# Performance work log

Hardware: AMD Instinct MI355X
Metric: run time of the kernel (lower is better)

The kernel has to match this reference:

```python
import jax, jax.numpy as jnp
import numpy as np

B, T, V, D, H, L = 256, 256, 128, 384, 6, 6
HS = D // H  # 64
FF = 4 * D


def _ln(x, g, b):
    m = jnp.mean(x, axis=-1, keepdims=True)
    v = jnp.var(x, axis=-1, keepdims=True)
    return (x - m) / jnp.sqrt(v + 1e-5) * g + b


def setup_inputs() -> dict:
    key = jax.random.key(0)
    ks = jax.random.split(key, 16)
    s = lambda k, sh: jax.random.normal(k, sh, dtype=jnp.float32) * 0.02
    return {
        "idx": jax.random.randint(ks[0], (B, T), 0, V),
        "tok_emb": s(ks[1], (V, D)),
        "pos_emb": s(ks[2], (T, D)),
        "Wq": s(ks[3], (L, H, D, HS)),
        "Wk": s(ks[4], (L, H, D, HS)),
        "Wv": s(ks[5], (L, H, D, HS)),
        "Wproj": s(ks[6], (L, D, D)),
        "bproj": jnp.zeros((L, D), jnp.float32),
        "ln1_g": jnp.ones((L, D), jnp.float32),
        "ln1_b": jnp.zeros((L, D), jnp.float32),
        "ln2_g": jnp.ones((L, D), jnp.float32),
        "ln2_b": jnp.zeros((L, D), jnp.float32),
        "W1": s(ks[7], (L, D, FF)),
        "b1": jnp.zeros((L, FF), jnp.float32),
        "W2": s(ks[8], (L, FF, D)),
        "b2": jnp.zeros((L, D), jnp.float32),
        "lnf_g": jnp.ones((D,), jnp.float32),
        "lnf_b": jnp.zeros((D,), jnp.float32),
        "Wlm": s(ks[9], (D, V)),
        "blm": jnp.zeros((V,), jnp.float32),
    }


def reference(idx, tok_emb, pos_emb, Wq, Wk, Wv, Wproj, bproj,
              ln1_g, ln1_b, ln2_g, ln2_b, W1, b1, W2, b2,
              lnf_g, lnf_b, Wlm, blm):
    Bv, Tv = idx.shape
    x = tok_emb[idx] + pos_emb[:Tv]  # [B,T,D]
    mask = jnp.tril(jnp.ones((Tv, Tv), dtype=bool))
    scale = HS ** -0.5
    for l in range(L):
        xn = _ln(x, ln1_g[l], ln1_b[l])
        q = jnp.einsum('btd,hdk->bhtk', xn, Wq[l])
        k = jnp.einsum('btd,hdk->bhtk', xn, Wk[l])
        v = jnp.einsum('btd,hdk->bhtk', xn, Wv[l])
        wei = jnp.einsum('bhtk,bhsk->bhts', q, k) * scale  # [B,H,T,T]
        wei = jnp.where(mask, wei, -jnp.inf)
        wei = jax.nn.softmax(wei, axis=-1)
        o = jnp.einsum('bhts,bhsk->bhtk', wei, v)
        o = o.transpose(0, 2, 1, 3).reshape(Bv, Tv, D)  # concat heads
        x = x + o @ Wproj[l] + bproj[l]
        xn = _ln(x, ln2_g[l], ln2_b[l])
        x = x + jax.nn.relu(xn @ W1[l] + b1[l]) @ W2[l] + b2[l]
    x = _ln(x, lnf_g, lnf_b)
    return x @ Wlm + blm  # logits [B,T,V]
```

## Files before the change

kernel.cpp:

```cpp
#include <hip/hip_runtime.h>
#include <stdint.h>

typedef unsigned short u16;
typedef __attribute__((ext_vector_type(8))) short short8;
typedef __attribute__((ext_vector_type(4))) float floatx4;

#define BB 256
#define TT 256
#define VOC 128
#define DD 384
#define HH 6
#define LLAY 6
#define HS 64
#define FFF 1536
#define BT (BB*TT)

__device__ __forceinline__ float b2f(u16 u) {
  union { float f; uint32_t i; } x; x.i = ((uint32_t)u) << 16; return x.f;
}
__device__ __forceinline__ u16 f2b(float f) {
  union { float f; uint32_t i; } x; x.f = f;
  uint32_t r = x.i + 0x7fffu + ((x.i >> 16) & 1u);
  return (u16)(r >> 16);
}
__device__ __forceinline__ float ldf(const void* p, size_t i, int bf) {
  return bf ? b2f(((const u16*)p)[i]) : ((const float*)p)[i];
}
__device__ __forceinline__ int get_bf(const u16* probe) {
  return probe[0] == 0x3F80;
}

__device__ __forceinline__ void gl2lds16(const u16* g, u16* l) {
  __builtin_amdgcn_global_load_lds(
      (const __attribute__((address_space(1))) unsigned int*)g,
      (__attribute__((address_space(3))) unsigned int*)l, 16, 0, 0);
}

__global__ __launch_bounds__(256) void k_repack_qkv(
    const void* __restrict__ Wq, const void* __restrict__ Wk,
    const void* __restrict__ Wv, u16* __restrict__ out,
    const void* __restrict__ g1, const void* __restrict__ b1n,
    float* __restrict__ u, float* __restrict__ v, const u16* probe) {
  __shared__ float t[32][33];
  int bf = get_bf(probe);
  int z = blockIdx.z;
  int h = z % 6, ls = z / 6, sel = ls % 3, l = ls / 3;
  const void* W = sel == 0 ? Wq : (sel == 1 ? Wk : Wv);
  int c0 = blockIdx.x * 32;
  int r0 = blockIdx.y * 32;
  int tx = threadIdx.x & 31, ty = threadIdx.x >> 5;
#pragma unroll
  for (int i = 0; i < 32; i += 8)
    t[ty + i][tx] = ldf(W, (((size_t)(l * 6 + h)) * 384 + r0 + ty + i) * 64 + c0 + tx, bf);
  __syncthreads();
  float gv = ldf(g1, (size_t)l * 384 + r0 + tx, bf);
  float bv = ldf(b1n, (size_t)l * 384 + r0 + tx, bf);
#pragma unroll
  for (int i = 0; i < 32; i += 8) {
    float w = t[tx][ty + i];
    int n = sel * 384 + h * 64 + c0 + ty + i;
    out[((size_t)l * 1152 + n) * 384 + r0 + tx] = f2b(w * gv);
    float pu = w * gv, pv = w * bv;
#pragma unroll
    for (int m = 1; m < 32; m <<= 1) { pu += __shfl_xor(pu, m); pv += __shfl_xor(pv, m); }
    if (tx == 0) {
      atomicAdd(&u[(size_t)l * 1152 + n], pu);
      atomicAdd(&v[(size_t)l * 1152 + n], pv);
    }
  }
}

__global__ __launch_bounds__(256) void k_transpose(
    const void* __restrict__ in, u16* __restrict__ out, int R, int C,
    const u16* probe) {
  __shared__ float t[32][33];
  int bf = get_bf(probe);
  int c0 = blockIdx.x * 32, r0 = blockIdx.y * 32, l = blockIdx.z;
  int tx = threadIdx.x & 31, ty = threadIdx.x >> 5;
  size_t base = (size_t)l * R * C;
#pragma unroll
  for (int i = 0; i < 32; i += 8)
    t[ty + i][tx] = ldf(in, base + (size_t)(r0 + ty + i) * C + c0 + tx, bf);
  __syncthreads();
#pragma unroll
  for (int i = 0; i < 32; i += 8)
    out[base + (size_t)(c0 + ty + i) * R + r0 + tx] = f2b(t[tx][ty + i]);
}

__global__ __launch_bounds__(256) void k_transpose_ln(
    const void* __restrict__ in, u16* __restrict__ out, int R, int C,
    const void* __restrict__ g, const void* __restrict__ b,
    float* __restrict__ u, float* __restrict__ v, const u16* probe) {
  __shared__ float t[32][33];
  int bf = get_bf(probe);
  int c0 = blockIdx.x * 32, r0 = blockIdx.y * 32, l = blockIdx.z;
  int tx = threadIdx.x & 31, ty = threadIdx.x >> 5;
  size_t base = (size_t)l * R * C;
#pragma unroll
  for (int i = 0; i < 32; i += 8)
    t[ty + i][tx] = ldf(in, base + (size_t)(r0 + ty + i) * C + c0 + tx, bf);
  __syncthreads();
  float gv = ldf(g, (size_t)l * R + r0 + tx, bf);
  float bv = ldf(b, (size_t)l * R + r0 + tx, bf);
#pragma unroll
  for (int i = 0; i < 32; i += 8) {
    float w = t[tx][ty + i];
    out[base + (size_t)(c0 + ty + i) * R + r0 + tx] = f2b(w * gv);
    float pu = w * gv, pv = w * bv;
#pragma unroll
    for (int m = 1; m < 32; m <<= 1) { pu += __shfl_xor(pu, m); pv += __shfl_xor(pv, m); }
    if (tx == 0) {
      atomicAdd(&u[(size_t)l * C + c0 + ty + i], pu);
      atomicAdd(&v[(size_t)l * C + c0 + ty + i], pv);
    }
  }
}

__global__ __launch_bounds__(256) void k_embed(
    const int* __restrict__ idx, const void* __restrict__ tok,
    const void* __restrict__ pos, u16* __restrict__ X,
    float* __restrict__ st, const u16* probe) {
  int bf = get_bf(probe);
  int gw = (blockIdx.x * 256 + threadIdx.x) >> 6;
  int lane = threadIdx.x & 63;
  int nw = (gridDim.x * 256) >> 6;
  for (int row = gw; row < BT; row += nw) {
    int v = idx[row];
    size_t tb = (size_t)v * DD, pb = (size_t)(row & 255) * DD;
    u16* xr = X + (size_t)row * DD;
    float s = 0.f, ss = 0.f;
#pragma unroll
    for (int i = 0; i < 6; ++i) {
      int d = i * 64 + lane;
      float x = ldf(tok, tb + d, bf) + ldf(pos, pb + d, bf);
      u16 xb = f2b(x);
      xr[d] = xb;
      float v2 = b2f(xb);
      s += v2; ss += v2 * v2;
    }
#pragma unroll
    for (int m = 1; m < 64; m <<= 1) { s += __shfl_xor(s, m); ss += __shfl_xor(ss, m); }
    if (lane == 0) {
      float mean = s * (1.f / DD);
      float var = ss * (1.f / DD) - mean * mean;
      st[2 * row] = mean;
      st[2 * row + 1] = rsqrtf(var + 1e-5f);
    }
  }
}

__global__ __launch_bounds__(256) void k_finstats(
    const float* __restrict__ stp, float* __restrict__ st) {
  int r = blockIdx.x * 256 + threadIdx.x;
  const float* p = stp + (size_t)r * 12;
  float s = 0.f, ss = 0.f;
#pragma unroll
  for (int k = 0; k < 6; ++k) { s += p[2 * k]; ss += p[2 * k + 1]; }
  float mean = s * (1.f / DD);
  float var = ss * (1.f / DD) - mean * mean;
  st[2 * r] = mean;
  st[2 * r + 1] = rsqrtf(var + 1e-5f);
}

template <int EPI>
__global__ __launch_bounds__(512) void k_gemm(
    const u16* __restrict__ A, const u16* __restrict__ Bt,
    const void* __restrict__ bias, int boff, u16* __restrict__ Xb,
    u16* __restrict__ C, float* __restrict__ Cf, int N, int K,
    const float* __restrict__ st, const float* __restrict__ u,
    const float* __restrict__ v, float* __restrict__ stp,
    const u16* probe) {
  __shared__ u16 As[256 * 64];
  __shared__ u16 Bs[128 * 64];
  int tid = threadIdx.x, lane = tid & 63, wave = tid >> 6;
  int m0 = blockIdx.x * 256, n0 = blockIdx.y * 128;
  int srow = tid >> 3;
  int skg = ((tid & 7) ^ (srow & 7)) * 8;
  const u16* gA = A + (size_t)(m0 + srow) * K + skg;
  const u16* gB = Bt + (size_t)(n0 + srow) * K + skg;
  u16* lA = As + wave * 512;
  u16* lB = Bs + wave * 512;
  int wy = wave >> 1, wx = wave & 1;
  int lr = lane & 15, quad = lane >> 4;
  int sx = lr & 7;
  floatx4 acc[4][4];
#pragma unroll
  for (int i = 0; i < 4; ++i)
#pragma unroll
    for (int j = 0; j < 4; ++j) acc[i][j] = (floatx4){0.f, 0.f, 0.f, 0.f};

  const u16* Abase = As + (size_t)(wy * 64 + lr) * 64;
  const u16* Bbase = Bs + (size_t)(wx * 64 + lr) * 64;

  int nk = K >> 6;
  for (int bk = 0; bk < nk; ++bk) {
    __syncthreads();
#pragma unroll
    for (int c = 0; c < 4; ++c)
      gl2lds16(gA + (size_t)(c * 64) * K, lA + c * 4096);
#pragma unroll
    for (int c = 0; c < 2; ++c)
      gl2lds16(gB + (size_t)(c * 64) * K, lB + c * 4096);
    gA += 64; gB += 64;
    __syncthreads();
#pragma unroll
    for (int half = 0; half < 2; ++half) {
      int ko = ((quad + half * 4) ^ sx) * 8;
      short8 af[4], bfr[4];
#pragma unroll
      for (int i = 0; i < 4; ++i) af[i] = *(const short8*)(Abase + i * 1024 + ko);
#pragma unroll
      for (int j = 0; j < 4; ++j) bfr[j] = *(const short8*)(Bbase + j * 1024 + ko);
#pragma unroll
      for (int i = 0; i < 4; ++i)
#pragma unroll
        for (int j = 0; j < 4; ++j)
          acc[i][j] = __builtin_amdgcn_mfma_f32_16x16x32_bf16(af[i], bfr[j], acc[i][j], 0, 0, 0);
    }
  }

  if (EPI == 2) {
    int bfl = get_bf(probe);
    float bv2[4];
#pragma unroll
    for (int j = 0; j < 4; ++j)
      bv2[j] = ldf(bias, boff + n0 + wx * 64 + j * 16 + lr, bfl);
    int slot = blockIdx.y * 2 + wx;
#pragma unroll
    for (int i = 0; i < 4; ++i) {
      int mrow = m0 + wy * 64 + i * 16 + quad * 4;
#pragma unroll
      for (int r = 0; r < 4; ++r) {
        int grow = mrow + r;
        float s = 0.f, ss = 0.f;
#pragma unroll
        for (int j = 0; j < 4; ++j) {
          int n = n0 + wx * 64 + j * 16 + lr;
          size_t off = (size_t)grow * N + n;
          u16 val = f2b(b2f(Xb[off]) + acc[i][j][r] + bv2[j]);
          Xb[off] = val;
          float yr = b2f(val);
          s += yr; ss += yr * yr;
        }
#pragma unroll
        for (int m = 1; m < 16; m <<= 1) { s += __shfl_xor(s, m); ss += __shfl_xor(ss, m); }
        if (lr == 0) {
          float2 pr; pr.x = s; pr.y = ss;
          *(float2*)(stp + ((size_t)grow * 6 + slot) * 2) = pr;
        }
      }
    }
  } else {
    int bfl = (EPI == 1 || EPI == 3) ? get_bf(probe) : 1;
    float un[4], vn[4], bv[4], sc[4];
    size_t sb[4]; int nc[4];
#pragma unroll
    for (int j = 0; j < 4; ++j) {
      int n = n0 + wx * 64 + j * 16 + lr;
      un[j] = u[n]; vn[j] = v[n];
      bv[j] = (EPI == 4) ? 0.f : ldf(bias, boff + n, bfl);
      sc[j] = 1.f;
      if (EPI == 4) {
        int sel = n >= 768 ? 2 : (n >= 384 ? 1 : 0);
        int hh = (n - sel * 384) >> 6;
        sb[j] = (size_t)sel * boff * 384 + (size_t)hh * boff * 64;
        nc[j] = n & 63;
        if (sel == 0) sc[j] = 0.125f;
      }
    }
#pragma unroll
    for (int i = 0; i < 4; ++i) {
      int mrow = m0 + wy * 64 + i * 16 + quad * 4;
#pragma unroll
      for (int r = 0; r < 4; ++r) {
        int grow = mrow + r;
        float mu = st[2 * grow], rs = st[2 * grow + 1];
#pragma unroll
        for (int j = 0; j < 4; ++j) {
          int n = n0 + wx * 64 + j * 16 + lr;
          float y = rs * (acc[i][j][r] - mu * un[j]) + vn[j];
          if (EPI == 1) C[(size_t)grow * N + n] = f2b(fmaxf(y + bv[j], 0.f));
          else if (EPI == 3) {
            if (bfl) C[(size_t)grow * N + n] = f2b(y + bv[j]);
            else Cf[(size_t)grow * N + n] = y + bv[j];
          } else {
            C[sb[j] + (size_t)grow * 64 + nc[j]] = f2b(y * sc[j]);
          }
        }
      }
    }
  }
}

__global__ __launch_bounds__(256) void k_attn(
    const u16* __restrict__ Q, const u16* __restrict__ K,
    const u16* __restrict__ V, u16* __restrict__ O, int TB) {
  __shared__ u16 Vt[2][64 * 72];
  __shared__ u16 P[4 * 16 * 72];
  int bx = blockIdx.x;
  int h = blockIdx.y;
  int b = blockIdx.z;
  int tid = threadIdx.x, lane = tid & 63, wave = tid >> 6;
  int lr = lane & 15, quad = lane >> 4;
  size_t hbase = (size_t)h * TB;
  const u16* Vb = V + (hbase + b * TT) * 64;

  int sp = tid & 31, sc = tid >> 5;

  {
    const u16* v0 = Vb + (size_t)(2 * sp) * 64 + sc * 8;
    short8 a = *(const short8*)(v0);
    short8 bvv = *(const short8*)(v0 + 64);
#pragma unroll
    for (int e = 0; e < 8; ++e) {
      uint32_t pk = (uint32_t)(u16)a[e] | ((uint32_t)(u16)bvv[e] << 16);
      *(uint32_t*)&Vt[0][(sc * 8 + e) * 72 + 2 * sp] = pk;
    }
  }

  int t0w = bx * 64 + wave * 16;
  const u16* qrow = Q + (hbase + b * TT + t0w + lr) * 64 + quad * 8;
  short8 qf0 = *(const short8*)(qrow);
  short8 qf1 = *(const short8*)(qrow + 32);

  float ls[4];
  floatx4 oacc[4];
#pragma unroll
  for (int r = 0; r < 4; ++r) ls[r] = 0.f;
#pragma unroll
  for (int j2 = 0; j2 < 4; ++j2) oacc[j2] = (floatx4){0.f, 0.f, 0.f, 0.f};
  u16* Pw = P + wave * 1152;
  const u16* Pr = P + wave * 1152 + lr * 72 + quad * 8;

  __syncthreads();

  for (int ks = 0; ks <= bx; ++ks) {
    short8 sva, svb;
    bool do_stage = (ks < bx);
    if (do_stage) {
      const u16* v0 = Vb + (size_t)((ks + 1) * 64 + 2 * sp) * 64 + sc * 8;
      sva = *(const short8*)(v0);
      svb = *(const short8*)(v0 + 64);
    }

    floatx4 s[4];
#pragma unroll
    for (int cc = 0; cc < 4; ++cc) s[cc] = (floatx4){0.f, 0.f, 0.f, 0.f};
    const u16* kbase = K + (hbase + b * TT + ks * 64 + lr) * 64 + quad * 8;
#pragma unroll
    for (int cc = 0; cc < 4; ++cc) {
      const u16* kr = kbase + cc * 16 * 64;
      short8 kf;
      kf = *(const short8*)(kr);      s[cc] = __builtin_amdgcn_mfma_f32_16x16x32_bf16(qf0, kf, s[cc], 0, 0, 0);
      kf = *(const short8*)(kr + 32); s[cc] = __builtin_amdgcn_mfma_f32_16x16x32_bf16(qf1, kf, s[cc], 0, 0, 0);
    }

    if (ks == bx) {
#pragma unroll
      for (int r = 0; r < 4; ++r) {
        int rowt = t0w + quad * 4 + r;
#pragma unroll
        for (int cc = 0; cc < 4; ++cc) {
          int c = ks * 64 + cc * 16 + lr;
          float e = (c > rowt) ? 0.f : __expf(s[cc][r]);
          ls[r] += e;
          Pw[(quad * 4 + r) * 72 + cc * 16 + lr] = f2b(e);
        }
      }
    } else {
#pragma unroll
      for (int r = 0; r < 4; ++r)
#pragma unroll
        for (int cc = 0; cc < 4; ++cc) {
          float e = __expf(s[cc][r]);
          ls[r] += e;
          Pw[(quad * 4 + r) * 72 + cc * 16 + lr] = f2b(e);
        }
    }
    asm volatile("s_waitcnt lgkmcnt(0)" ::: "memory");
    const u16* Vc = &Vt[ks & 1][0];
#pragma unroll
    for (int h2 = 0; h2 < 2; ++h2) {
      short8 pf = *(const short8*)(Pr + h2 * 32);
#pragma unroll
      for (int j2 = 0; j2 < 4; ++j2) {
        short8 vf = *(const short8*)(Vc + (j2 * 16 + lr) * 72 + h2 * 32 + quad * 8);
        oacc[j2] = __builtin_amdgcn_mfma_f32_16x16x32_bf16(pf, vf, oacc[j2], 0, 0, 0);
      }
    }

    if (do_stage) {
      u16* dst = &Vt[(ks + 1) & 1][0];
#pragma unroll
      for (int e = 0; e < 8; ++e) {
        uint32_t pk = (uint32_t)(u16)sva[e] | ((uint32_t)(u16)svb[e] << 16);
        *(uint32_t*)&dst[(sc * 8 + e) * 72 + 2 * sp] = pk;
      }
    }
    __syncthreads();
  }

#pragma unroll
  for (int r = 0; r < 4; ++r) {
#pragma unroll
    for (int mm = 1; mm < 16; mm <<= 1) ls[r] += __shfl_xor(ls[r], mm);
    ls[r] = 1.f / ls[r];
  }

  u16* Ot = (u16*)Vt;
#pragma unroll
  for (int j2 = 0; j2 < 4; ++j2)
#pragma unroll
    for (int r = 0; r < 4; ++r)
      Ot[(wave * 16 + quad * 4 + r) * 72 + j2 * 16 + lr] = f2b(oacc[j2][r] * ls[r]);
  __syncthreads();
#pragma unroll
  for (int p = 0; p < 2; ++p) {
    int row = p * 32 + (tid >> 3), cg = tid & 7;
    short8 o8 = *(const short8*)(Ot + row * 72 + cg * 8);
    *(short8*)(O + (size_t)(b * TT + bx * 64 + row) * DD + h * 64 + cg * 8) = o8;
  }
}

extern "C" void kernel_launch(void* const* d_in, const int* in_sizes, int n_in,
                              void* d_out, int out_size, void* d_ws, size_t ws_size,
                              hipStream_t stream) {
  const int* idx   = (const int*)d_in[0];
  const void* tok  = d_in[1];
  const void* pos  = d_in[2];
  const void* Wq   = d_in[3];
  const void* Wk   = d_in[4];
  const void* Wv   = d_in[5];
  const void* Wproj= d_in[6];
  const void* bproj= d_in[7];
  const void* ln1g = d_in[8];
  const void* ln1b = d_in[9];
  const void* ln2g = d_in[10];
  const void* ln2b = d_in[11];
  const void* W1   = d_in[12];
  const void* b1   = d_in[13];
  const void* W2   = d_in[14];
  const void* b2   = d_in[15];
  const void* lnfg = d_in[16];
  const void* lnfb = d_in[17];
  const void* Wlm  = d_in[18];
  const void* blm  = d_in[19];
  const u16* probe = (const u16*)d_in[8];

  char* ws = (char*)d_ws;
  u16* X  = (u16*)ws;
  u16* XA = (u16*)(ws + 50331648);
  char* wb = ws + 100663296;
  u16* Wqkv_t  = (u16*)wb;
  u16* Wproj_t = (u16*)(wb + 5308416);
  u16* W1_t    = (u16*)(wb + 7077888);
  u16* W2_t    = (u16*)(wb + 14155776);
  u16* Wlm_t   = (u16*)(wb + 21233664);
  char* uvb = wb + 21331968;
  float* u_qkv = (float*)uvb;
  float* v_qkv = (float*)(uvb + 27648);
  float* u_fc1 = (float*)(uvb + 55296);
  float* v_fc1 = (float*)(uvb + 92160);
  float* u_lm  = (float*)(uvb + 129024);
  float* v_lm  = (float*)(uvb + 129536);
  float* st    = (float*)(uvb + 130048);
  float* stp   = (float*)(uvb + 130048 + 524288);
  const size_t fixed = 100663296 + 21331968 + 130048 + 524288 + 3145728;
  u16* S  = (u16*)(ws + fixed);

  size_t avail = ws_size > fixed ? ws_size - fixed : 0;
  int nA = 8, nM = 8;
  if ((size_t)BT * 1152 * 2 <= avail) nA = 1;
  else if ((size_t)(BT / 2) * 1152 * 2 <= avail) nA = 2;
  else if ((size_t)(BT / 4) * 1152 * 2 <= avail) nA = 4;
  if ((size_t)BT * 1536 * 2 <= avail) nM = 1;
  else if ((size_t)(BT / 2) * 1536 * 2 <= avail) nM = 2;
  else if ((size_t)(BT / 4) * 1536 * 2 <= avail) nM = 4;
  const int rowsA = BT / nA;
  const int rowsM = BT / nM;

  hipMemsetAsync(uvb, 0, 130048, stream);
  { dim3 g(2, 12, 108);
    k_repack_qkv<<<g, 256, 0, stream>>>(Wq, Wk, Wv, Wqkv_t, ln1g, ln1b,
                                        u_qkv, v_qkv, probe); }
  { dim3 g(12, 12, 6);   k_transpose<<<g, 256, 0, stream>>>(Wproj, Wproj_t, 384, 384, probe); }
  { dim3 g(48, 12, 6);
    k_transpose_ln<<<g, 256, 0, stream>>>(W1, W1_t, 384, 1536, ln2g, ln2b,
                                          u_fc1, v_fc1, probe); }
  { dim3 g(12, 48, 6);   k_transpose<<<g, 256, 0, stream>>>(W2, W2_t, 1536, 384, probe); }
  { dim3 g(4, 12, 1);
    k_transpose_ln<<<g, 256, 0, stream>>>(Wlm, Wlm_t, 384, 128, lnfg, lnfb,
                                          u_lm, v_lm, probe); }

  k_embed<<<2048, 256, 0, stream>>>(idx, tok, pos, X, st, probe);

  for (int l = 0; l < LLAY; ++l) {
    for (int c = 0; c < nA; ++c) {
      const u16* A0c = X + (size_t)c * rowsA * DD;
      { dim3 g(rowsA / 256, 9);
        k_gemm<4><<<g, 512, 0, stream>>>(A0c, Wqkv_t + (size_t)l * 1152 * 384,
                                         nullptr, rowsA, nullptr, S, nullptr, 1152, 384,
                                         st + (size_t)2 * c * rowsA,
                                         u_qkv + l * 1152, v_qkv + l * 1152,
                                         nullptr, probe); }
      { dim3 g(4, HH, rowsA / 256);
        k_attn<<<g, 256, 0, stream>>>(S, S + (size_t)6 * rowsA * 64,
                                      S + (size_t)12 * rowsA * 64,
                                      XA + (size_t)c * rowsA * DD, rowsA); }
    }
    { dim3 g(256, 3);
      k_gemm<2><<<g, 512, 0, stream>>>(XA, Wproj_t + (size_t)l * 384 * 384,
                                       bproj, l * 384, X, nullptr, nullptr, 384, 384,
                                       nullptr, nullptr, nullptr, stp, probe); }
    k_finstats<<<BT / 256, 256, 0, stream>>>(stp, st);
    for (int c = 0; c < nM; ++c) {
      const u16* A0c = X + (size_t)c * rowsM * DD;
      { dim3 g(rowsM / 256, 12);
        k_gemm<1><<<g, 512, 0, stream>>>(A0c, W1_t + (size_t)l * 1536 * 384,
                                         b1, l * 1536, nullptr, S, nullptr, 1536, 384,
                                         st + (size_t)2 * c * rowsM,
                                         u_fc1 + l * 1536, v_fc1 + l * 1536,
                                         nullptr, probe); }
      { dim3 g(rowsM / 256, 3);
        k_gemm<2><<<g, 512, 0, stream>>>(S, W2_t + (size_t)l * 384 * 1536,
                                         b2, l * 384, X + (size_t)c * rowsM * DD,
                                         nullptr, nullptr, 384, 1536,
                                         nullptr, nullptr, nullptr,
                                         stp + (size_t)c * rowsM * 12, probe); }
    }
    k_finstats<<<BT / 256, 256, 0, stream>>>(stp, st);
  }
  { dim3 g(256, 1);
    k_gemm<3><<<g, 512, 0, stream>>>(X, Wlm_t, blm, 0, nullptr,
                                     (u16*)d_out, (float*)d_out, 128, 384,
                                     st, u_lm, v_lm, nullptr, probe); }
}
```

Measured before the change: 3.136 ms.

## Fuse LayerNorm stat finalization into GEMM prologue and prefetch K tiles in attention

Removes the separate k_finstats kernel by having each consuming GEMM block reduce the per-row partial sums into shared memory at its start. The embed kernel now writes partial sums in the same layout. The attention kernel also double-buffers K fragments in registers, loading the next key tile while computing the current one. This saves kernel launches and a global round-trip for stats. In exchange, the partial reduction is repeated in every column block and register pressure in attention rises.

```diff
diff --git a/kernel.cpp b/kernel.cpp
--- a/kernel.cpp
+++ b/kernel.cpp
@@ -119,7 +119,7 @@
 __global__ __launch_bounds__(256) void k_embed(
     const int* __restrict__ idx, const void* __restrict__ tok,
     const void* __restrict__ pos, u16* __restrict__ X,
-    float* __restrict__ st, const u16* probe) {
+    float* __restrict__ stp, const u16* probe) {
   int bf = get_bf(probe);
   int gw = (blockIdx.x * 256 + threadIdx.x) >> 6;
   int lane = threadIdx.x & 63;
@@ -140,26 +140,13 @@
     }
 #pragma unroll
     for (int m = 1; m < 64; m <<= 1) { s += __shfl_xor(s, m); ss += __shfl_xor(ss, m); }
-    if (lane == 0) {
-      float mean = s * (1.f / DD);
-      float var = ss * (1.f / DD) - mean * mean;
-      st[2 * row] = mean;
-      st[2 * row + 1] = rsqrtf(var + 1e-5f);
-    }
-  }
-}
-
-__global__ __launch_bounds__(256) void k_finstats(
-    const float* __restrict__ stp, float* __restrict__ st) {
-  int r = blockIdx.x * 256 + threadIdx.x;
-  const float* p = stp + (size_t)r * 12;
-  float s = 0.f, ss = 0.f;
-#pragma unroll
-  for (int k = 0; k < 6; ++k) { s += p[2 * k]; ss += p[2 * k + 1]; }
-  float mean = s * (1.f / DD);
-  float var = ss * (1.f / DD) - mean * mean;
-  st[2 * r] = mean;
-  st[2 * r + 1] = rsqrtf(var + 1e-5f);
+    if (lane < 6) {
+      float2 pr;
+      pr.x = (lane == 0) ? s : 0.f;
+      pr.y = (lane == 0) ? ss : 0.f;
+      *(float2*)(stp + (size_t)row * 12 + lane * 2) = pr;
+    }
+  }
 }
 
 template <int EPI>
@@ -167,13 +154,27 @@
     const u16* __restrict__ A, const u16* __restrict__ Bt,
     const void* __restrict__ bias, int boff, u16* __restrict__ Xb,
     u16* __restrict__ C, float* __restrict__ Cf, int N, int K,
-    const float* __restrict__ st, const float* __restrict__ u,
-    const float* __restrict__ v, float* __restrict__ stp,
-    const u16* probe) {
+    const float* __restrict__ u, const float* __restrict__ v,
+    float* __restrict__ stp, const u16* probe) {
   __shared__ u16 As[256 * 64];
   __shared__ u16 Bs[128 * 64];
+  __shared__ float stl[256][2];
   int tid = threadIdx.x, lane = tid & 63, wave = tid >> 6;
   int m0 = blockIdx.x * 256, n0 = blockIdx.y * 128;
+
+  if (EPI != 2) {
+    if (tid < 256) {
+      const float* p = stp + (size_t)(m0 + tid) * 12;
+      float s = 0.f, ss = 0.f;
+#pragma unroll
+      for (int k2 = 0; k2 < 6; ++k2) { s += p[2 * k2]; ss += p[2 * k2 + 1]; }
+      float mean = s * (1.f / DD);
+      float var = ss * (1.f / DD) - mean * mean;
+      stl[tid][0] = mean;
+      stl[tid][1] = rsqrtf(var + 1e-5f);
+    }
+  }
+
   int srow = tid >> 3;
   int skg = ((tid & 7) ^ (srow & 7)) * 8;
   const u16* gA = A + (size_t)(m0 + srow) * K + skg;
@@ -270,11 +271,12 @@
     }
 #pragma unroll
     for (int i = 0; i < 4; ++i) {
-      int mrow = m0 + wy * 64 + i * 16 + quad * 4;
+      int lrow0 = wy * 64 + i * 16 + quad * 4;
 #pragma unroll
       for (int r = 0; r < 4; ++r) {
-        int grow = mrow + r;
-        float mu = st[2 * grow], rs = st[2 * grow + 1];
+        int lrow = lrow0 + r;
+        int grow = m0 + lrow;
+        float mu = stl[lrow][0], rs = stl[lrow][1];
 #pragma unroll
         for (int j = 0; j < 4; ++j) {
           int n = n0 + wx * 64 + j * 16 + lr;
@@ -323,6 +325,14 @@
   short8 qf0 = *(const short8*)(qrow);
   short8 qf1 = *(const short8*)(qrow + 32);
 
+  const u16* kbase0 = K + (hbase + b * TT + lr) * 64 + quad * 8;
+  short8 kc[8];
+#pragma unroll
+  for (int cc = 0; cc < 4; ++cc) {
+    kc[2 * cc]     = *(const short8*)(kbase0 + cc * 16 * 64);
+    kc[2 * cc + 1] = *(const short8*)(kbase0 + cc * 16 * 64 + 32);
+  }
+
   float ls[4];
   floatx4 oacc[4];
 #pragma unroll
@@ -335,9 +345,15 @@
   __syncthreads();
 
   for (int ks = 0; ks <= bx; ++ks) {
-    short8 sva, svb;
+    short8 kn[8], sva, svb;
     bool do_stage = (ks < bx);
     if (do_stage) {
+      const u16* kb2 = kbase0 + (size_t)(ks + 1) * 64 * 64;
+#pragma unroll
+      for (int cc = 0; cc < 4; ++cc) {
+        kn[2 * cc]     = *(const short8*)(kb2 + cc * 16 * 64);
+        kn[2 * cc + 1] = *(const short8*)(kb2 + cc * 16 * 64 + 32);
+      }
       const u16* v0 = Vb + (size_t)((ks + 1) * 64 + 2 * sp) * 64 + sc * 8;
       sva = *(const short8*)(v0);
       svb = *(const short8*)(v0 + 64);
@@ -346,13 +362,10 @@
     floatx4 s[4];
 #pragma unroll
     for (int cc = 0; cc < 4; ++cc) s[cc] = (floatx4){0.f, 0.f, 0.f, 0.f};
-    const u16* kbase = K + (hbase + b * TT + ks * 64 + lr) * 64 + quad * 8;
 #pragma unroll
     for (int cc = 0; cc < 4; ++cc) {
-      const u16* kr = kbase + cc * 16 * 64;
-      short8 kf;
-      kf = *(const short8*)(kr);      s[cc] = __builtin_amdgcn_mfma_f32_16x16x32_bf16(qf0, kf, s[cc], 0, 0, 0);
-      kf = *(const short8*)(kr + 32); s[cc] = __builtin_amdgcn_mfma_f32_16x16x32_bf16(qf1, kf, s[cc], 0, 0, 0);
+      s[cc] = __builtin_amdgcn_mfma_f32_16x16x32_bf16(qf0, kc[2 * cc], s[cc], 0, 0, 0);
+      s[cc] = __builtin_amdgcn_mfma_f32_16x16x32_bf16(qf1, kc[2 * cc + 1], s[cc], 0, 0, 0);
     }
 
     if (ks == bx) {
@@ -396,6 +409,8 @@
         uint32_t pk = (uint32_t)(u16)sva[e] | ((uint32_t)(u16)svb[e] << 16);
         *(uint32_t*)&dst[(sc * 8 + e) * 72 + 2 * sp] = pk;
       }
+#pragma unroll
+      for (int e = 0; e < 8; ++e) kc[e] = kn[e];
     }
     __syncthreads();
   }
@@ -463,7 +478,6 @@
   float* v_fc1 = (float*)(uvb + 92160);
   float* u_lm  = (float*)(uvb + 129024);
   float* v_lm  = (float*)(uvb + 129536);
-  float* st    = (float*)(uvb + 130048);
   float* stp   = (float*)(uvb + 130048 + 524288);
   const size_t fixed = 100663296 + 21331968 + 130048 + 524288 + 3145728;
   u16* S  = (u16*)(ws + fixed);
@@ -492,7 +506,7 @@
     k_transpose_ln<<<g, 256, 0, stream>>>(Wlm, Wlm_t, 384, 128, lnfg, lnfb,
                                           u_lm, v_lm, probe); }
 
-  k_embed<<<2048, 256, 0, stream>>>(idx, tok, pos, X, st, probe);
+  k_embed<<<2048, 256, 0, stream>>>(idx, tok, pos, X, stp, probe);
 
   for (int l = 0; l < LLAY; ++l) {
     for (int c = 0; c < nA; ++c) {
@@ -500,9 +514,8 @@
       { dim3 g(rowsA / 256, 9);
         k_gemm<4><<<g, 512, 0, stream>>>(A0c, Wqkv_t + (size_t)l * 1152 * 384,
                                          nullptr, rowsA, nullptr, S, nullptr, 1152, 384,
-                                         st + (size_t)2 * c * rowsA,
                                          u_qkv + l * 1152, v_qkv + l * 1152,
-                                         nullptr, probe); }
+                                         stp + (size_t)c * rowsA * 12, probe); }
       { dim3 g(4, HH, rowsA / 256);
         k_attn<<<g, 256, 0, stream>>>(S, S + (size_t)6 * rowsA * 64,
                                       S + (size_t)12 * rowsA * 64,
@@ -511,27 +524,24 @@
     { dim3 g(256, 3);
       k_gemm<2><<<g, 512, 0, stream>>>(XA, Wproj_t + (size_t)l * 384 * 384,
                                        bproj, l * 384, X, nullptr, nullptr, 384, 384,
-                                       nullptr, nullptr, nullptr, stp, probe); }
-    k_finstats<<<BT / 256, 256, 0, stream>>>(stp, st);
+                                       nullptr, nullptr, stp, probe); }
     for (int c = 0; c < nM; ++c) {
       const u16* A0c = X + (size_t)c * rowsM * DD;
       { dim3 g(rowsM / 256, 12);
         k_gemm<1><<<g, 512, 0, stream>>>(A0c, W1_t + (size_t)l * 1536 * 384,
                                          b1, l * 1536, nullptr, S, nullptr, 1536, 384,
-                                         st + (size_t)2 * c * rowsM,
                                          u_fc1 + l * 1536, v_fc1 + l * 1536,
-                                         nullptr, probe); }
+                                         stp + (size_t)c * rowsM * 12, probe); }
       { dim3 g(rowsM / 256, 3);
         k_gemm<2><<<g, 512, 0, stream>>>(S, W2_t + (size_t)l * 384 * 1536,
                                          b2, l * 384, X + (size_t)c * rowsM * DD,
                                          nullptr, nullptr, 384, 1536,
-                                         nullptr, nullptr, nullptr,
+                                         nullptr, nullptr,
                                          stp + (size_t)c * rowsM * 12, probe); }
     }
-    k_finstats<<<BT / 256, 256, 0, stream>>>(stp, st);
   }
   { dim3 g(256, 1);
     k_gemm<3><<<g, 512, 0, stream>>>(X, Wlm_t, blm, 0, nullptr,
                                      (u16*)d_out, (float*)d_out, 128, 384,
-                                     st, u_lm, v_lm, nullptr, probe); }
-}
+                                     u_lm, v_lm, stp, probe); }
+}
```

After: 3.108 ms. Within noise of the previous version (-0.9%).
